# Kernel tuning notes

Hardware: AMD Instinct MI355X
Metric: run time of the kernel (lower is better)

The kernel has to match this reference:

```python
import jax, jax.numpy as jnp
import numpy as np

B, S, D = 2, 2048, 1024
H, DK = 16, 64          # heads, d_k (= d_v)
DH = 4096               # FFN hidden
EPS = 1e-5


def _layer_norm(x, gamma, beta):
    mu = jnp.mean(x, axis=-1, keepdims=True)
    var = jnp.var(x, axis=-1, keepdims=True)
    return (x - mu) * jax.lax.rsqrt(var + EPS) * gamma + beta


def setup_inputs() -> dict:
    key = jax.random.key(0)
    ks = jax.random.split(key, 8)
    s = lambda fan_in: 1.0 / np.sqrt(fan_in)
    return {
        "x": jax.random.normal(ks[0], (B, S, D), dtype=jnp.float32),
        # NOTE: source module uses W_q for queries, keys AND values (bug kept faithfully),
        # so W_k / W_v are never used and are not materialized.
        "Wq": jax.random.normal(ks[1], (D, H * DK), dtype=jnp.float32) * s(D),
        "bq": jnp.zeros((H * DK,), dtype=jnp.float32),
        "Wo": jax.random.normal(ks[2], (H * DK, D), dtype=jnp.float32) * s(H * DK),
        "bo": jnp.zeros((D,), dtype=jnp.float32),
        "ln1_g": jnp.ones((D,), dtype=jnp.float32),
        "ln1_b": jnp.zeros((D,), dtype=jnp.float32),
        "W1": jax.random.normal(ks[3], (D, DH), dtype=jnp.float32) * s(D),
        "b1": jnp.zeros((DH,), dtype=jnp.float32),
        "W2": jax.random.normal(ks[4], (DH, D), dtype=jnp.float32) * s(DH),
        "b2": jnp.zeros((D,), dtype=jnp.float32),
        "ln2_g": jnp.ones((D,), dtype=jnp.float32),
        "ln2_b": jnp.zeros((D,), dtype=jnp.float32),
    }


def reference(x, Wq, bq, Wo, bo, ln1_g, ln1_b, W1, b1, W2, b2, ln2_g, ln2_b):
    residual = x
    # projections: q, k, v all use W_q (faithful to source)
    q = (x @ Wq + bq).reshape(B, S, H, DK)
    k = (x @ Wq + bq).reshape(B, S, H, DK)
    v = (x @ Wq + bq).reshape(B, S, H, DK)
    # scores scaled by sqrt(sequence_length), as in the source
    scale = 1.0 / jnp.sqrt(jnp.float32(S))
    scores = jnp.einsum("bqhd,bkhd->bhqk", q, k) * scale
    probs = jax.nn.softmax(scores, axis=-1)
    attn = jnp.einsum("bhqk,bkhd->bqhd", probs, v).reshape(B, S, H * DK)
    attn = attn @ Wo + bo
    # dropout is identity in eval mode
    x = _layer_norm(attn + residual, ln1_g, ln1_b)
    residual = x
    h = jax.nn.relu(x @ W1 + b1)
    x = h @ W2 + b2
    x = _layer_norm(x + residual, ln2_g, ln2_b)
    return x
```

## Files before the change

kernel.cpp:

```cpp
#include <hip/hip_runtime.h>
#include <stdint.h>


typedef unsigned short u16;
typedef __attribute__((ext_vector_type(8))) short v8s;
typedef __attribute__((ext_vector_type(4))) float v4f;

#define AS1 __attribute__((address_space(1)))
#define AS3 __attribute__((address_space(3)))

__device__ __forceinline__ void gl_lds16(const u16* g, u16* l) {
  __builtin_amdgcn_global_load_lds((const AS1 void*)g, (AS3 void*)l, 16, 0, 0);
}

__device__ __forceinline__ float bf2f(u16 u) {
  union { uint32_t i; float f; } v; v.i = ((uint32_t)u) << 16; return v.f;
}
__device__ __forceinline__ u16 f2bf(float f) {
  union { float f; uint32_t i; } v; v.f = f;
  uint32_t x = v.i;
  return (u16)((x + 0x7FFFu + ((x >> 16) & 1u)) >> 16);
}
__device__ __forceinline__ uint32_t fbits(float f) {
  union { float f; uint32_t u; } v; v.f = f; return v.u;
}

__global__ __launch_bounds__(256) void cvt_f2b(
    const float* __restrict__ src, u16* __restrict__ dst, int n4) {
  int i = (blockIdx.x * 256 + threadIdx.x);
  if (i < n4) {
    float4 v = *(const float4*)(src + (size_t)i * 4);
    ushort4 o;
    o.x = f2bf(v.x); o.y = f2bf(v.y); o.z = f2bf(v.z); o.w = f2bf(v.w);
    *(ushort4*)(dst + (size_t)i * 4) = o;
  }
}

__global__ __launch_bounds__(256) void transpose_f2b(
    const float* __restrict__ src, u16* __restrict__ dst,
    int R, int C, int ld_s, int ld_d) {
  __shared__ float tile[32][33];
  const int tx = threadIdx.x & 31, ty = threadIdx.x >> 5;
  const int c0 = blockIdx.x * 32, r0 = blockIdx.y * 32;
#pragma unroll
  for (int j = 0; j < 32; j += 8)
    tile[ty + j][tx] = src[(size_t)(r0 + ty + j) * ld_s + c0 + tx];
  __syncthreads();
#pragma unroll
  for (int j = 0; j < 32; j += 8)
    dst[(size_t)(c0 + ty + j) * ld_d + r0 + tx] = f2bf(tile[tx][ty + j]);
}

__global__ __launch_bounds__(256) void transpose_b2b(
    const u16* __restrict__ src, u16* __restrict__ dst,
    int R, int C, int ld_s, int ld_d) {
  __shared__ u16 tile[32][33];
  const int tx = threadIdx.x & 31, ty = threadIdx.x >> 5;
  const int c0 = blockIdx.x * 32, r0 = blockIdx.y * 32;
#pragma unroll
  for (int j = 0; j < 32; j += 8)
    tile[ty + j][tx] = src[(size_t)(r0 + ty + j) * ld_s + c0 + tx];
  __syncthreads();
#pragma unroll
  for (int j = 0; j < 32; j += 8)
    dst[(size_t)(c0 + ty + j) * ld_d + r0 + tx] = tile[tx][ty + j];
}

__global__ __launch_bounds__(256) void gemm_g1(
    const u16* __restrict__ A, const u16* __restrict__ Bt,
    const float* __restrict__ bias, void* __restrict__ C,
    int M, int N, int K, int relu, int out_f32) {
  __shared__ u16 As[2][4096];
  __shared__ u16 Bs[2][4096];
  const int tid = threadIdx.x;
  const int w = tid >> 6, l = tid & 63;
  const int lane16 = l & 15, kgrp = l >> 4;
  const int m0 = blockIdx.y * 128, n0 = blockIdx.x * 128;
  const int wr = (w >> 1) * 64, wc = (w & 1) * 64;

  const int sr = w * 32 + (l >> 2);
  const int sc = l & 3;
  const int sgc = sc ^ ((sr & 3) ^ ((sr >> 2) & 3));
  const u16* gA = A + (size_t)(m0 + sr) * K + 8 * sgc;
  const u16* gB = Bt + (size_t)(n0 + sr) * K + 8 * sgc;
  const size_t rstep = (size_t)16 * K;
  const int fl = (lane16 & 3) ^ ((lane16 >> 2) & 3);

  v4f acc[4][4];
#pragma unroll
  for (int i = 0; i < 4; i++)
#pragma unroll
    for (int j = 0; j < 4; j++)
#pragma unroll
      for (int r = 0; r < 4; r++) acc[i][j][r] = 0.f;

  gl_lds16(gA, &As[0][w * 1024]);
  gl_lds16(gA + rstep, &As[0][w * 1024 + 512]);
  gl_lds16(gB, &Bs[0][w * 1024]);
  gl_lds16(gB + rstep, &Bs[0][w * 1024 + 512]);

  int cur = 0;
  for (int k0 = 0; k0 < K; k0 += 32) {
    __syncthreads();
    if (k0 + 32 < K) {
      int nxt = cur ^ 1;
      gl_lds16(gA + k0 + 32, &As[nxt][w * 1024]);
      gl_lds16(gA + k0 + 32 + rstep, &As[nxt][w * 1024 + 512]);
      gl_lds16(gB + k0 + 32, &Bs[nxt][w * 1024]);
      gl_lds16(gB + k0 + 32 + rstep, &Bs[nxt][w * 1024 + 512]);
    }
    v8s a[4], b[4];
#pragma unroll
    for (int mi = 0; mi < 4; mi++)
      a[mi] = *(const v8s*)(&As[cur][(wr + mi * 16 + lane16) * 32 + 8 * (kgrp ^ fl)]);
#pragma unroll
    for (int ni = 0; ni < 4; ni++)
      b[ni] = *(const v8s*)(&Bs[cur][(wc + ni * 16 + lane16) * 32 + 8 * (kgrp ^ fl)]);
#pragma unroll
    for (int mi = 0; mi < 4; mi++)
#pragma unroll
      for (int ni = 0; ni < 4; ni++)
        acc[mi][ni] = __builtin_amdgcn_mfma_f32_16x16x32_bf16(a[mi], b[ni], acc[mi][ni], 0, 0, 0);
    cur ^= 1;
  }

#pragma unroll
  for (int ni = 0; ni < 4; ni++) {
    int col = n0 + wc + ni * 16 + lane16;
    float bv = bias ? bias[col] : 0.f;
#pragma unroll
    for (int mi = 0; mi < 4; mi++) {
      int row = m0 + wr + mi * 16 + kgrp * 4;
#pragma unroll
      for (int r = 0; r < 4; r++) {
        float v = acc[mi][ni][r] + bv;
        if (relu) v = fmaxf(v, 0.f);
        size_t idx = (size_t)(row + r) * N + col;
        if (out_f32) ((float*)C)[idx] = v;
        else ((u16*)C)[idx] = f2bf(v);
      }
    }
  }
}

__global__ __launch_bounds__(256) void gemm_g2(
    const u16* __restrict__ A, const u16* __restrict__ Bt,
    const float* __restrict__ bias, void* __restrict__ C,
    int M, int N, int K, int relu, int accum, int out_f32) {
  __shared__ u16 As[2][8192];
  __shared__ u16 Bs[2][4096];
  const int tid = threadIdx.x;
  const int w = tid >> 6, l = tid & 63;
  const int l16 = l & 15, kgrp = l >> 4;
  const int m0 = blockIdx.y * 128, n0 = blockIdx.x * 64;
  const int wr = (w >> 1) * 64, wc = (w & 1) * 32;

  const int srow = w * 8 + (l >> 3);
  const u16* gA[4];
#pragma unroll
  for (int i = 0; i < 4; i++) {
    int r = i * 32 + srow;
    gA[i] = A + (size_t)(m0 + r) * K + 8 * ((l & 7) ^ (r & 7));
  }
  const u16* gB[2];
#pragma unroll
  for (int i = 0; i < 2; i++) {
    int r = i * 32 + srow;
    gB[i] = Bt + (size_t)(n0 + r) * K + 8 * ((l & 7) ^ (r & 7));
  }

  v4f acc[4][2];
#pragma unroll
  for (int i = 0; i < 4; i++)
#pragma unroll
    for (int j = 0; j < 2; j++)
#pragma unroll
      for (int r = 0; r < 4; r++) acc[i][j][r] = 0.f;

#pragma unroll
  for (int i = 0; i < 4; i++) gl_lds16(gA[i], &As[0][(i * 256 + w * 64) * 8]);
#pragma unroll
  for (int i = 0; i < 2; i++) gl_lds16(gB[i], &Bs[0][(i * 256 + w * 64) * 8]);

  int cur = 0;
  for (int k0 = 0; k0 < K; k0 += 64) {
    __syncthreads();
    if (k0 + 64 < K) {
      int nxt = cur ^ 1;
#pragma unroll
      for (int i = 0; i < 4; i++)
        gl_lds16(gA[i] + k0 + 64, &As[nxt][(i * 256 + w * 64) * 8]);
#pragma unroll
      for (int i = 0; i < 2; i++)
        gl_lds16(gB[i] + k0 + 64, &Bs[nxt][(i * 256 + w * 64) * 8]);
    }
    v8s a[4][2], b[2][2];
#pragma unroll
    for (int ks = 0; ks < 2; ks++) {
      int ch = 8 * ((ks * 4 + kgrp) ^ (l16 & 7));
#pragma unroll
      for (int mi = 0; mi < 4; mi++)
        a[mi][ks] = *(const v8s*)(&As[cur][(wr + mi * 16 + l16) * 64 + ch]);
#pragma unroll
      for (int ni = 0; ni < 2; ni++)
        b[ni][ks] = *(const v8s*)(&Bs[cur][(wc + ni * 16 + l16) * 64 + ch]);
    }
#pragma unroll
    for (int ks = 0; ks < 2; ks++)
#pragma unroll
      for (int mi = 0; mi < 4; mi++)
#pragma unroll
        for (int ni = 0; ni < 2; ni++)
          acc[mi][ni] = __builtin_amdgcn_mfma_f32_16x16x32_bf16(a[mi][ks], b[ni][ks], acc[mi][ni], 0, 0, 0);
    cur ^= 1;
  }

#pragma unroll
  for (int ni = 0; ni < 2; ni++) {
    int col = n0 + wc + ni * 16 + l16;
    float bv = bias ? bias[col] : 0.f;
#pragma unroll
    for (int mi = 0; mi < 4; mi++) {
      int row = m0 + wr + mi * 16 + kgrp * 4;
#pragma unroll
      for (int r = 0; r < 4; r++) {
        float v = acc[mi][ni][r] + bv;
        if (relu) v = fmaxf(v, 0.f);
        size_t idx = (size_t)(row + r) * N + col;
        if (out_f32) {
          float* Cf = (float*)C;
          if (accum) v += Cf[idx];
          Cf[idx] = v;
        } else {
          ((u16*)C)[idx] = f2bf(v);
        }
      }
    }
  }
}

__global__ __launch_bounds__(256) void gemm_g2s(
    const u16* __restrict__ A, const u16* __restrict__ Bt,
    const float* __restrict__ bias, void* __restrict__ C0,
    u16* __restrict__ C1, int M, int N, int ldk, int klen, int c0_f32) {
  __shared__ u16 As[2][8192];
  __shared__ u16 Bs[2][4096];
  const int tid = threadIdx.x;
  const int w = tid >> 6, l = tid & 63;
  const int l16 = l & 15, kgrp = l >> 4;
  const int m0 = blockIdx.y * 128, n0 = blockIdx.x * 64;
  const int z = blockIdx.z;
  const int k_begin = z * klen;
  const int wr = (w >> 1) * 64, wc = (w & 1) * 32;

  const int srow = w * 8 + (l >> 3);
  const u16* gA[4];
#pragma unroll
  for (int i = 0; i < 4; i++) {
    int r = i * 32 + srow;
    gA[i] = A + (size_t)(m0 + r) * ldk + k_begin + 8 * ((l & 7) ^ (r & 7));
  }
  const u16* gB[2];
#pragma unroll
  for (int i = 0; i < 2; i++) {
    int r = i * 32 + srow;
    gB[i] = Bt + (size_t)(n0 + r) * ldk + k_begin + 8 * ((l & 7) ^ (r & 7));
  }

  v4f acc[4][2];
#pragma unroll
  for (int i = 0; i < 4; i++)
#pragma unroll
    for (int j = 0; j < 2; j++)
#pragma unroll
      for (int r = 0; r < 4; r++) acc[i][j][r] = 0.f;

#pragma unroll
  for (int i = 0; i < 4; i++) gl_lds16(gA[i], &As[0][(i * 256 + w * 64) * 8]);
#pragma unroll
  for (int i = 0; i < 2; i++) gl_lds16(gB[i], &Bs[0][(i * 256 + w * 64) * 8]);

  int cur = 0;
  for (int k0 = 0; k0 < klen; k0 += 64) {
    __syncthreads();
    if (k0 + 64 < klen) {
      int nxt = cur ^ 1;
#pragma unroll
      for (int i = 0; i < 4; i++)
        gl_lds16(gA[i] + k0 + 64, &As[nxt][(i * 256 + w * 64) * 8]);
#pragma unroll
      for (int i = 0; i < 2; i++)
        gl_lds16(gB[i] + k0 + 64, &Bs[nxt][(i * 256 + w * 64) * 8]);
    }
    v8s a[4][2], b[2][2];
#pragma unroll
    for (int ks = 0; ks < 2; ks++) {
      int ch = 8 * ((ks * 4 + kgrp) ^ (l16 & 7));
#pragma unroll
      for (int mi = 0; mi < 4; mi++)
        a[mi][ks] = *(const v8s*)(&As[cur][(wr + mi * 16 + l16) * 64 + ch]);
#pragma unroll
      for (int ni = 0; ni < 2; ni++)
        b[ni][ks] = *(const v8s*)(&Bs[cur][(wc + ni * 16 + l16) * 64 + ch]);
    }
#pragma unroll
    for (int ks = 0; ks < 2; ks++)
#pragma unroll
      for (int mi = 0; mi < 4; mi++)
#pragma unroll
        for (int ni = 0; ni < 2; ni++)
          acc[mi][ni] = __builtin_amdgcn_mfma_f32_16x16x32_bf16(a[mi][ks], b[ni][ks], acc[mi][ni], 0, 0, 0);
    cur ^= 1;
  }

#pragma unroll
  for (int ni = 0; ni < 2; ni++) {
    int col = n0 + wc + ni * 16 + l16;
    float bv = (bias && z == 0) ? bias[col] : 0.f;
#pragma unroll
    for (int mi = 0; mi < 4; mi++) {
      int row = m0 + wr + mi * 16 + kgrp * 4;
#pragma unroll
      for (int r = 0; r < 4; r++) {
        float v = acc[mi][ni][r] + bv;
        size_t idx = (size_t)(row + r) * N + col;
        if (z == 0) {
          if (c0_f32) ((float*)C0)[idx] = v;
          else ((u16*)C0)[idx] = f2bf(v);
        } else {
          C1[idx] = f2bf(v);
        }
      }
    }
  }
}

__global__ __launch_bounds__(256) void attn_kernel(
    const u16* __restrict__ Q, const u16* __restrict__ Qt,
    u16* __restrict__ O) {
  __shared__ u16 KV[2][8192];
  __shared__ __align__(16) u16 Ps[4][2304];
  const int tid = threadIdx.x;
  const int w = tid >> 6, l = tid & 63;
  const int l16 = l & 15, kgrp = l >> 4;
  const int bh = blockIdx.y, b = bh >> 4, h = bh & 15;
  const int q0 = blockIdx.x * 128;
  const size_t rowQ = (size_t)(b * 2048 + q0 + w * 32);
  const float cexp = 1.4426950408889634f / 45.254833995939045f;

  const int srow = w * 8 + (l >> 3);
  const int sch8 = 8 * ((l & 7) ^ (srow & 7));
  const u16* gK0 = Q + (size_t)(b * 2048 + srow) * 1024 + h * 64 + sch8;
  const u16* gK1 = gK0 + (size_t)32 * 1024;
  const u16* gV0 = Qt + (size_t)(h * 64 + srow) * 4096 + b * 2048 + sch8;
  const u16* gV1 = gV0 + (size_t)32 * 4096;

  v8s qb[2][2];
#pragma unroll
  for (int nj = 0; nj < 2; nj++)
#pragma unroll
    for (int ks = 0; ks < 2; ks++) {
      v8s t = *(const v8s*)(Q + (rowQ + nj * 16 + l16) * 1024 + h * 64 + ks * 32 + kgrp * 8);
#pragma unroll
      for (int j = 0; j < 8; j++) t[j] = (short)f2bf(bf2f((u16)t[j]) * cexp);
      qb[nj][ks] = t;
    }

  v4f o[2][4];
  float ls[2] = {0.f, 0.f};
#pragma unroll
  for (int i = 0; i < 2; i++)
#pragma unroll
    for (int j = 0; j < 4; j++)
#pragma unroll
      for (int r = 0; r < 4; r++) o[i][j][r] = 0.f;

  gl_lds16(gK0, &KV[0][w * 512]);
  gl_lds16(gK1, &KV[0][2048 + w * 512]);
  gl_lds16(gV0, &KV[0][4096 + w * 512]);
  gl_lds16(gV1, &KV[0][4096 + 2048 + w * 512]);

  u16* Pw = &Ps[w][0];
  int cur = 0;
  for (int kb = 0; kb < 2048; kb += 64) {
    __syncthreads();
    if (kb + 64 < 2048) {
      int nxt = cur ^ 1;
      gl_lds16(gK0 + (size_t)(kb + 64) * 1024, &KV[nxt][w * 512]);
      gl_lds16(gK1 + (size_t)(kb + 64) * 1024, &KV[nxt][2048 + w * 512]);
      gl_lds16(gV0 + (kb + 64), &KV[nxt][4096 + w * 512]);
      gl_lds16(gV1 + (kb + 64), &KV[nxt][4096 + 2048 + w * 512]);
    }
    const u16* Ks = &KV[cur][0];
    const u16* Vt = &KV[cur][4096];

    v4f st[4][2];
#pragma unroll
    for (int i = 0; i < 4; i++)
#pragma unroll
      for (int j = 0; j < 2; j++)
#pragma unroll
        for (int r = 0; r < 4; r++) st[i][j][r] = 0.f;
#pragma unroll
    for (int ks = 0; ks < 2; ks++) {
      v8s ka[4];
#pragma unroll
      for (int mi = 0; mi < 4; mi++)
        ka[mi] = *(const v8s*)(Ks + (mi * 16 + l16) * 64 + 8 * ((ks * 4 + kgrp) ^ (l16 & 7)));
#pragma unroll
      for (int mi = 0; mi < 4; mi++)
#pragma unroll
        for (int nj = 0; nj < 2; nj++)
          st[mi][nj] = __builtin_amdgcn_mfma_f32_16x16x32_bf16(ka[mi], qb[nj][ks], st[mi][nj], 0, 0, 0);
    }

#pragma unroll
    for (int mi = 0; mi < 4; mi++)
#pragma unroll
      for (int nj = 0; nj < 2; nj++) {
        float p0 = __builtin_amdgcn_exp2f(st[mi][nj][0]);
        float p1 = __builtin_amdgcn_exp2f(st[mi][nj][1]);
        float p2 = __builtin_amdgcn_exp2f(st[mi][nj][2]);
        float p3 = __builtin_amdgcn_exp2f(st[mi][nj][3]);
        ls[nj] += (p0 + p1) + (p2 + p3);
        uint2 pk;
        pk.x = __builtin_amdgcn_perm(fbits(p1), fbits(p0), 0x07060302u);
        pk.y = __builtin_amdgcn_perm(fbits(p3), fbits(p2), 0x07060302u);
        *(uint2*)(Pw + (nj * 16 + l16) * 72 + mi * 16 + kgrp * 4) = pk;
      }

#pragma unroll
    for (int t = 0; t < 2; t++) {
      v8s pa[2], vb[4];
#pragma unroll
      for (int nj = 0; nj < 2; nj++)
        pa[nj] = *(const v8s*)(Pw + (nj * 16 + l16) * 72 + t * 32 + kgrp * 8);
#pragma unroll
      for (int ni = 0; ni < 4; ni++)
        vb[ni] = *(const v8s*)(Vt + (ni * 16 + l16) * 64 + 8 * ((t * 4 + kgrp) ^ (l16 & 7)));
#pragma unroll
      for (int nj = 0; nj < 2; nj++)
#pragma unroll
        for (int ni = 0; ni < 4; ni++)
          o[nj][ni] = __builtin_amdgcn_mfma_f32_16x16x32_bf16(pa[nj], vb[ni], o[nj][ni], 0, 0, 0);
    }
    cur ^= 1;
  }

#pragma unroll
  for (int nj = 0; nj < 2; nj++) {
    float t = ls[nj];
    t += __shfl_xor(t, 16, 64);
    t += __shfl_xor(t, 32, 64);
    ls[nj] = t;
  }

#pragma unroll
  for (int nj = 0; nj < 2; nj++) {
#pragma unroll
    for (int r = 0; r < 4; r++) {
      float den = __shfl(ls[nj], kgrp * 4 + r, 64);
      float rden = 1.f / den;
#pragma unroll
      for (int ni = 0; ni < 4; ni++) {
        O[(rowQ + nj * 16 + kgrp * 4 + r) * 1024 + h * 64 + ni * 16 + l16] =
            f2bf(o[nj][ni][r] * rden);
      }
    }
  }
}

__global__ __launch_bounds__(256) void ln_residual(
    const void* __restrict__ Y, const void* __restrict__ Y2,
    const void* __restrict__ Xr,
    const float* __restrict__ g, const float* __restrict__ bb,
    void* __restrict__ out, int yf, int y2f, int xf, int of) {
  const int row = blockIdx.x, tid = threadIdx.x;
  const size_t base = (size_t)row * 1024;
  float v[4], s = 0.f, sq = 0.f;
#pragma unroll
  for (int i = 0; i < 4; i++) {
    int c = tid + i * 256;
    float ya = yf ? ((const float*)Y)[base + c] : bf2f(((const u16*)Y)[base + c]);
    float xa = xf ? ((const float*)Xr)[base + c] : bf2f(((const u16*)Xr)[base + c]);
    float x = ya + xa;
    if (Y2) {
      float y2a = y2f ? ((const float*)Y2)[base + c] : bf2f(((const u16*)Y2)[base + c]);
      x += y2a;
    }
    v[i] = x; s += x; sq += x * x;
  }
#pragma unroll
  for (int off = 32; off >= 1; off >>= 1) {
    s += __shfl_down(s, off, 64);
    sq += __shfl_down(sq, off, 64);
  }
  __shared__ float rs[4], rq[4];
  const int w = tid >> 6, l = tid & 63;
  if (l == 0) { rs[w] = s; rq[w] = sq; }
  __syncthreads();
  s = rs[0] + rs[1] + rs[2] + rs[3];
  sq = rq[0] + rq[1] + rq[2] + rq[3];
  const float mu = s * (1.f / 1024.f);
  const float var = sq * (1.f / 1024.f) - mu * mu;
  const float rstd = rsqrtf(var + 1e-5f);
#pragma unroll
  for (int i = 0; i < 4; i++) {
    int c = tid + i * 256;
    float r = (v[i] - mu) * rstd * g[c] + bb[c];
    if (of) ((float*)out)[base + c] = r;
    else ((u16*)out)[base + c] = f2bf(r);
  }
}

extern "C" void kernel_launch(void* const* d_in, const int* in_sizes, int n_in,
                              void* d_out, int out_size, void* d_ws, size_t ws_size,
                              hipStream_t stream) {
  const float* x   = (const float*)d_in[0];
  const float* Wq  = (const float*)d_in[1];
  const float* bq  = (const float*)d_in[2];
  const float* Wo  = (const float*)d_in[3];
  const float* bo  = (const float*)d_in[4];
  const float* g1  = (const float*)d_in[5];
  const float* be1 = (const float*)d_in[6];
  const float* W1  = (const float*)d_in[7];
  const float* b1  = (const float*)d_in[8];
  const float* W2  = (const float*)d_in[9];
  const float* b2  = (const float*)d_in[10];
  const float* g2  = (const float*)d_in[11];
  const float* be2 = (const float*)d_in[12];
  float* out = (float*)d_out;
  u16* ws  = (u16*)d_ws;

  const size_t M1 = 1048576;
  dim3 blk(256);
  const bool big = ws_size >= (size_t)37 * M1 * 2;

  if (big) {
    u16* xb   = ws + 0;
    u16* Qb   = ws + 4 * M1;
    u16* Qt   = ws + 8 * M1;
    u16* WqT  = ws + 12 * M1;
    u16* W1T  = ws + 13 * M1;
    u16* W2T  = ws + 17 * M1;
    u16* Hh   = ws + 21 * M1;
    u16* attn = xb;  u16* Yb = Qt;  u16* x1 = Qb;  u16* WoT = WqT;
    u16* P1wo = W1T;
    u16* P1f2 = Qt;

    cvt_f2b<<<dim3(4096), blk, 0, stream>>>(x, xb, 1048576);
    transpose_f2b<<<dim3(32, 32), blk, 0, stream>>>(Wq, WqT, 1024, 1024, 1024, 1024);
    gemm_g2<<<dim3(16, 32), blk, 0, stream>>>(xb, WqT, bq, Qb, 4096, 1024, 1024, 0, 0, 0);

    transpose_b2b<<<dim3(32, 128), blk, 0, stream>>>(Qb, Qt, 4096, 1024, 1024, 4096);
    attn_kernel<<<dim3(16, 32), blk, 0, stream>>>(Qb, Qt, attn);

    transpose_f2b<<<dim3(32, 32), blk, 0, stream>>>(Wo, WoT, 1024, 1024, 1024, 1024);
    gemm_g2s<<<dim3(16, 32, 2), blk, 0, stream>>>(attn, WoT, bo, Yb, P1wo,
                                                  4096, 1024, 1024, 512, 0);
    ln_residual<<<dim3(4096), blk, 0, stream>>>(Yb, P1wo, x, g1, be1, x1, 0, 0, 1, 0);

    transpose_f2b<<<dim3(128, 32), blk, 0, stream>>>(W1, W1T, 1024, 4096, 4096, 1024);
    gemm_g1<<<dim3(32, 32), blk, 0, stream>>>(x1, W1T, b1, Hh, 4096, 4096, 1024, 1, 0);

    transpose_f2b<<<dim3(32, 128), blk, 0, stream>>>(W2, W2T, 4096, 1024, 1024, 4096);
    gemm_g2s<<<dim3(16, 32, 2), blk, 0, stream>>>(Hh, W2T, b2, out, P1f2,
                                                  4096, 1024, 4096, 2048, 1);

    ln_residual<<<dim3(4096), blk, 0, stream>>>(out, P1f2, x1, g2, be2, out, 1, 0, 0, 1);
  } else {
    u16* xb   = ws + 0;
    u16* Qb   = ws + 4 * M1;
    u16* Qt   = ws + 8 * M1;
    u16* attn = xb;  u16* Yb = Qt;  u16* x1 = Qb;  u16* Hc = xb;
    u16* Wt1  = ws + 12 * M1;
    u16* Wt2  = ws + 13 * M1;

    cvt_f2b<<<dim3(4096), blk, 0, stream>>>(x, xb, 1048576);
    transpose_f2b<<<dim3(32, 32), blk, 0, stream>>>(Wq, Wt1, 1024, 1024, 1024, 1024);
    gemm_g2<<<dim3(16, 32), blk, 0, stream>>>(xb, Wt1, bq, Qb, 4096, 1024, 1024, 0, 0, 0);

    transpose_b2b<<<dim3(32, 128), blk, 0, stream>>>(Qb, Qt, 4096, 1024, 1024, 4096);
    attn_kernel<<<dim3(16, 32), blk, 0, stream>>>(Qb, Qt, attn);

    transpose_f2b<<<dim3(32, 32), blk, 0, stream>>>(Wo, Wt2, 1024, 1024, 1024, 1024);
    gemm_g2<<<dim3(16, 32), blk, 0, stream>>>(attn, Wt2, bo, Yb, 4096, 1024, 1024, 0, 0, 0);
    ln_residual<<<dim3(4096), blk, 0, stream>>>(Yb, nullptr, x, g1, be1, x1, 0, 0, 1, 0);

    for (int c = 0; c < 4; c++) {
      transpose_f2b<<<dim3(32, 32), blk, 0, stream>>>(W1 + (size_t)c * 1024, Wt1,
                                                      1024, 1024, 4096, 1024);
      gemm_g2<<<dim3(16, 32), blk, 0, stream>>>(x1, Wt1, b1 + (size_t)c * 1024, Hc,
                                                4096, 1024, 1024, 1, 0, 0);
      transpose_f2b<<<dim3(32, 32), blk, 0, stream>>>(W2 + (size_t)c * M1, Wt2,
                                                      1024, 1024, 1024, 1024);
      gemm_g2<<<dim3(16, 32), blk, 0, stream>>>(Hc, Wt2, (c == 0) ? b2 : (const float*)nullptr,
                                                out, 4096, 1024, 1024, 0, (c > 0) ? 1 : 0, 1);
    }
    ln_residual<<<dim3(4096), blk, 0, stream>>>(out, nullptr, x1, g2, be2, out, 1, 0, 0, 1);
  }
}
```

Before: 355.9 us.

## Merge weight prep into one kernel and split FFN2 GEMM four ways over K

Combines the x conversion and the Wq, W1 and W2 transposes into a single prep launch, cutting launch count and letting those independent pieces run together. The second FFN GEMM switches from a 2-way to a 4-way split-K with 128x128 tiles. Three of the four partials are stored in bf16, and a new final layernorm kernel sums them with the residual. This adds parallelism and block count for the K=4096 GEMM, at the cost of more partial-sum traffic and extra bf16 rounding of the partials.

```diff
diff --git a/kernel.cpp b/kernel.cpp
--- a/kernel.cpp
+++ b/kernel.cpp
@@ -23,6 +23,42 @@
 }
 __device__ __forceinline__ uint32_t fbits(float f) {
   union { float f; uint32_t u; } v; v.f = f; return v.u;
+}
+
+__global__ __launch_bounds__(256) void prep(
+    const float* __restrict__ x, u16* __restrict__ xb,
+    const float* __restrict__ Wq, u16* __restrict__ WqT,
+    const float* __restrict__ W1, u16* __restrict__ W1T,
+    const float* __restrict__ W2, u16* __restrict__ W2T) {
+  const int id = blockIdx.x;
+  if (id < 4096) {
+    int i = id * 256 + threadIdx.x;
+    float4 v = *(const float4*)(x + (size_t)i * 4);
+    ushort4 o;
+    o.x = f2bf(v.x); o.y = f2bf(v.y); o.z = f2bf(v.z); o.w = f2bf(v.w);
+    *(ushort4*)(xb + (size_t)i * 4) = o;
+    return;
+  }
+  __shared__ float tile[32][33];
+  const float* src; u16* dst; int ld_s, ld_d, r0, c0;
+  if (id < 5120) {
+    int t = id - 4096; src = Wq; dst = WqT; ld_s = 1024; ld_d = 1024;
+    c0 = (t & 31) * 32; r0 = (t >> 5) * 32;
+  } else if (id < 9216) {
+    int t = id - 5120; src = W1; dst = W1T; ld_s = 4096; ld_d = 1024;
+    c0 = (t & 127) * 32; r0 = (t >> 7) * 32;
+  } else {
+    int t = id - 9216; src = W2; dst = W2T; ld_s = 1024; ld_d = 4096;
+    c0 = (t & 31) * 32; r0 = (t >> 5) * 32;
+  }
+  const int tx = threadIdx.x & 31, ty = threadIdx.x >> 5;
+#pragma unroll
+  for (int j = 0; j < 32; j += 8)
+    tile[ty + j][tx] = src[(size_t)(r0 + ty + j) * ld_s + c0 + tx];
+  __syncthreads();
+#pragma unroll
+  for (int j = 0; j < 32; j += 8)
+    dst[(size_t)(c0 + ty + j) * ld_d + r0 + tx] = f2bf(tile[tx][ty + j]);
 }
 
 __global__ __launch_bounds__(256) void cvt_f2b(
@@ -138,6 +174,86 @@
         size_t idx = (size_t)(row + r) * N + col;
         if (out_f32) ((float*)C)[idx] = v;
         else ((u16*)C)[idx] = f2bf(v);
+      }
+    }
+  }
+}
+
+__global__ __launch_bounds__(256) void gemm_g1s(
+    const u16* __restrict__ A, const u16* __restrict__ Bt,
+    const float* __restrict__ bias, float* __restrict__ C0,
+    u16* __restrict__ P1, u16* __restrict__ P2, u16* __restrict__ P3,
+    int M, int N, int ldk, int klen) {
+  __shared__ u16 As[2][4096];
+  __shared__ u16 Bs[2][4096];
+  const int tid = threadIdx.x;
+  const int w = tid >> 6, l = tid & 63;
+  const int lane16 = l & 15, kgrp = l >> 4;
+  const int m0 = blockIdx.y * 128, n0 = blockIdx.x * 128;
+  const int z = blockIdx.z;
+  const int k_begin = z * klen;
+  const int wr = (w >> 1) * 64, wc = (w & 1) * 64;
+
+  const int sr = w * 32 + (l >> 2);
+  const int sc = l & 3;
+  const int sgc = sc ^ ((sr & 3) ^ ((sr >> 2) & 3));
+  const u16* gA = A + (size_t)(m0 + sr) * ldk + k_begin + 8 * sgc;
+  const u16* gB = Bt + (size_t)(n0 + sr) * ldk + k_begin + 8 * sgc;
+  const size_t rstep = (size_t)16 * ldk;
+  const int fl = (lane16 & 3) ^ ((lane16 >> 2) & 3);
+
+  v4f acc[4][4];
+#pragma unroll
+  for (int i = 0; i < 4; i++)
+#pragma unroll
+    for (int j = 0; j < 4; j++)
+#pragma unroll
+      for (int r = 0; r < 4; r++) acc[i][j][r] = 0.f;
+
+  gl_lds16(gA, &As[0][w * 1024]);
+  gl_lds16(gA + rstep, &As[0][w * 1024 + 512]);
+  gl_lds16(gB, &Bs[0][w * 1024]);
+  gl_lds16(gB + rstep, &Bs[0][w * 1024 + 512]);
+
+  int cur = 0;
+  for (int k0 = 0; k0 < klen; k0 += 32) {
+    __syncthreads();
+    if (k0 + 32 < klen) {
+      int nxt = cur ^ 1;
+      gl_lds16(gA + k0 + 32, &As[nxt][w * 1024]);
+      gl_lds16(gA + k0 + 32 + rstep, &As[nxt][w * 1024 + 512]);
+      gl_lds16(gB + k0 + 32, &Bs[nxt][w * 1024]);
+      gl_lds16(gB + k0 + 32 + rstep, &Bs[nxt][w * 1024 + 512]);
+    }
+    v8s a[4], b[4];
+#pragma unroll
+    for (int mi = 0; mi < 4; mi++)
+      a[mi] = *(const v8s*)(&As[cur][(wr + mi * 16 + lane16) * 32 + 8 * (kgrp ^ fl)]);
+#pragma unroll
+    for (int ni = 0; ni < 4; ni++)
+      b[ni] = *(const v8s*)(&Bs[cur][(wc + ni * 16 + lane16) * 32 + 8 * (kgrp ^ fl)]);
+#pragma unroll
+    for (int mi = 0; mi < 4; mi++)
+#pragma unroll
+      for (int ni = 0; ni < 4; ni++)
+        acc[mi][ni] = __builtin_amdgcn_mfma_f32_16x16x32_bf16(a[mi], b[ni], acc[mi][ni], 0, 0, 0);
+    cur ^= 1;
+  }
+
+  u16* Pz = (z == 1) ? P1 : ((z == 2) ? P2 : P3);
+#pragma unroll
+  for (int ni = 0; ni < 4; ni++) {
+    int col = n0 + wc + ni * 16 + lane16;
+    float bv = (bias && z == 0) ? bias[col] : 0.f;
+#pragma unroll
+    for (int mi = 0; mi < 4; mi++) {
+      int row = m0 + wr + mi * 16 + kgrp * 4;
+#pragma unroll
+      for (int r = 0; r < 4; r++) {
+        float v = acc[mi][ni][r] + bv;
+        size_t idx = (size_t)(row + r) * N + col;
+        if (z == 0) C0[idx] = v;
+        else Pz[idx] = f2bf(v);
       }
     }
   }
@@ -510,6 +626,43 @@
     float r = (v[i] - mu) * rstd * g[c] + bb[c];
     if (of) ((float*)out)[base + c] = r;
     else ((u16*)out)[base + c] = f2bf(r);
+  }
+}
+
+__global__ __launch_bounds__(256) void ln_final5(
+    const float* __restrict__ Y0, const u16* __restrict__ P1,
+    const u16* __restrict__ P2, const u16* __restrict__ P3,
+    const u16* __restrict__ x1,
+    const float* __restrict__ g, const float* __restrict__ bb,
+    float* __restrict__ out) {
+  const int row = blockIdx.x, tid = threadIdx.x;
+  const size_t base = (size_t)row * 1024;
+  float v[4], s = 0.f, sq = 0.f;
+#pragma unroll
+  for (int i = 0; i < 4; i++) {
+    int c = tid + i * 256;
+    float x = Y0[base + c] + bf2f(P1[base + c]) + bf2f(P2[base + c]) +
+              bf2f(P3[base + c]) + bf2f(x1[base + c]);
+    v[i] = x; s += x; sq += x * x;
+  }
+#pragma unroll
+  for (int off = 32; off >= 1; off >>= 1) {
+    s += __shfl_down(s, off, 64);
+    sq += __shfl_down(sq, off, 64);
+  }
+  __shared__ float rs[4], rq[4];
+  const int w = tid >> 6, l = tid & 63;
+  if (l == 0) { rs[w] = s; rq[w] = sq; }
+  __syncthreads();
+  s = rs[0] + rs[1] + rs[2] + rs[3];
+  sq = rq[0] + rq[1] + rq[2] + rq[3];
+  const float mu = s * (1.f / 1024.f);
+  const float var = sq * (1.f / 1024.f) - mu * mu;
+  const float rstd = rsqrtf(var + 1e-5f);
+#pragma unroll
+  for (int i = 0; i < 4; i++) {
+    int c = tid + i * 256;
+    out[base + c] = (v[i] - mu) * rstd * g[c] + bb[c];
   }
 }
 
@@ -545,13 +698,12 @@
     u16* W2T  = ws + 17 * M1;
     u16* Hh   = ws + 21 * M1;
     u16* attn = xb;  u16* Yb = Qt;  u16* x1 = Qb;  u16* WoT = WqT;
-    u16* P1wo = W1T;
-    u16* P1f2 = Qt;
-
-    cvt_f2b<<<dim3(4096), blk, 0, stream>>>(x, xb, 1048576);
-    transpose_f2b<<<dim3(32, 32), blk, 0, stream>>>(Wq, WqT, 1024, 1024, 1024, 1024);
+    u16* P1wo = Qb;
+    u16* P1 = Qt;  u16* P2 = xb;  u16* P3 = W1T;
+
+    prep<<<dim3(13312), blk, 0, stream>>>(x, xb, Wq, WqT, W1, W1T, W2, W2T);
+
     gemm_g2<<<dim3(16, 32), blk, 0, stream>>>(xb, WqT, bq, Qb, 4096, 1024, 1024, 0, 0, 0);
-
     transpose_b2b<<<dim3(32, 128), blk, 0, stream>>>(Qb, Qt, 4096, 1024, 1024, 4096);
     attn_kernel<<<dim3(16, 32), blk, 0, stream>>>(Qb, Qt, attn);
 
@@ -560,14 +712,11 @@
                                                   4096, 1024, 1024, 512, 0);
     ln_residual<<<dim3(4096), blk, 0, stream>>>(Yb, P1wo, x, g1, be1, x1, 0, 0, 1, 0);
 
-    transpose_f2b<<<dim3(128, 32), blk, 0, stream>>>(W1, W1T, 1024, 4096, 4096, 1024);
     gemm_g1<<<dim3(32, 32), blk, 0, stream>>>(x1, W1T, b1, Hh, 4096, 4096, 1024, 1, 0);
 
-    transpose_f2b<<<dim3(32, 128), blk, 0, stream>>>(W2, W2T, 4096, 1024, 1024, 4096);
-    gemm_g2s<<<dim3(16, 32, 2), blk, 0, stream>>>(Hh, W2T, b2, out, P1f2,
-                                                  4096, 1024, 4096, 2048, 1);
-
-    ln_residual<<<dim3(4096), blk, 0, stream>>>(out, P1f2, x1, g2, be2, out, 1, 0, 0, 1);
+    gemm_g1s<<<dim3(8, 32, 4), blk, 0, stream>>>(Hh, W2T, b2, out, P1, P2, P3,
+                                                 4096, 1024, 4096, 1024);
+    ln_final5<<<dim3(4096), blk, 0, stream>>>(out, P1, P2, P3, x1, g2, be2, out);
   } else {
     u16* xb   = ws + 0;
     u16* Qb   = ws + 4 * M1;
```

Result: no change. 357.4 us (+0.4%).
